# Optimization experiments

Measured on AMD Instinct MI355X. Metric: run time of the kernel, lower is better.

The kernel has to match this reference:

```python
import jax, jax.numpy as jnp
import numpy as np
from jax import lax

V, B, C, H, W, D, G_DEF = 5, 2, 32, 128, 160, 32, 8


def _combine(proj):
    # proj: [B,2,4,4]; [:,0]=extrinsic, [:,1]=intrinsic; new[:, :3, :4] = K[:3,:3] @ E[:3,:4]
    ext, K = proj[:, 0], proj[:, 1]
    top = jnp.einsum('bij,bjk->bik', K[:, :3, :3], ext[:, :3, :4])
    return ext.at[:, :3, :4].set(top)


def _bilinear(img, x, y):
    # img [C,H,W]; x,y [N] pixel coords; zeros padding, align_corners=True (torch grid_sample)
    Ch, Hh, Wh = img.shape
    x0 = jnp.floor(x); y0 = jnp.floor(y)
    wx1 = x - x0; wy1 = y - y0
    def gather(xi, yi):
        valid = ((xi >= 0) & (xi <= Wh - 1) & (yi >= 0) & (yi <= Hh - 1)).astype(img.dtype)
        xc = jnp.clip(xi, 0, Wh - 1).astype(jnp.int32)
        yc = jnp.clip(yi, 0, Hh - 1).astype(jnp.int32)
        return img[:, yc, xc] * valid
    return (gather(x0, y0) * ((1 - wx1) * (1 - wy1)) + gather(x0 + 1, y0) * (wx1 * (1 - wy1))
            + gather(x0, y0 + 1) * ((1 - wx1) * wy1) + gather(x0 + 1, y0 + 1) * (wx1 * wy1))


def _conv3d(x, w, b, pad):
    y = lax.conv_general_dilated(x, w, (1, 1, 1), [(pad, pad)] * 3,
                                 dimension_numbers=('NCDHW', 'OIDHW', 'NCDHW'))
    return y + b[None, :, None, None, None]


def setup_inputs():
    key = jax.random.key(0)
    ks = jax.random.split(key, 8)
    features = jax.random.normal(ks[0], (V, B, C, H, W), jnp.float32)
    pm = np.zeros((B, V, 2, 4, 4), np.float32)
    for v in range(V):
        E = np.eye(4, dtype=np.float32); E[0, 3] = 0.05 * v  # small baseline along x
        K = np.eye(4, dtype=np.float32)
        K[0, 0] = K[1, 1] = float(W); K[0, 2] = W / 2.0; K[1, 2] = H / 2.0
        pm[:, v, 0] = E; pm[:, v, 1] = K
    proj_matrices = jnp.asarray(pm)
    d = jnp.linspace(1.0, 3.0, D, dtype=jnp.float32)
    depth_values = jnp.broadcast_to(d[None, :, None, None], (B, D, H, W))
    s = 0.1
    reg_w1 = jax.random.normal(ks[1], (8, G_DEF, 3, 3, 3), jnp.float32) * s
    reg_b1 = jnp.zeros((8,), jnp.float32)
    reg_w2 = jax.random.normal(ks[2], (1, 8, 3, 3, 3), jnp.float32) * s
    reg_b2 = jnp.zeros((1,), jnp.float32)
    pw_w1 = jax.random.normal(ks[3], (16, 1, 1, 1, 1), jnp.float32) * s
    pw_b1 = jnp.zeros((16,), jnp.float32)
    pw_w2 = jax.random.normal(ks[4], (8, 16, 1, 1, 1), jnp.float32) * s
    pw_b2 = jnp.zeros((8,), jnp.float32)
    pw_w3 = jax.random.normal(ks[5], (1, 8, 1, 1, 1), jnp.float32) * s
    pw_b3 = jnp.zeros((1,), jnp.float32)
    return dict(features=features, proj_matrices=proj_matrices, depth_values=depth_values,
                reg_w1=reg_w1, reg_b1=reg_b1, reg_w2=reg_w2, reg_b2=reg_b2,
                pw_w1=pw_w1, pw_b1=pw_b1, pw_w2=pw_w2, pw_b2=pw_b2,
                pw_w3=pw_w3, pw_b3=pw_b3, num_depth=D, G=G_DEF)


def reference(features, proj_matrices, depth_values, reg_w1, reg_b1, reg_w2, reg_b2,
              pw_w1, pw_b1, pw_w2, pw_b2, pw_w3, pw_b3, num_depth, G):
    Vn, Bn, Cn, Hn, Wn = features.shape
    Dn = num_depth
    ref_fea = features[0].reshape(Bn, G, Cn // G, Hn, Wn)
    ref_proj = _combine(proj_matrices[:, 0])
    ref_proj_inv = jnp.linalg.inv(ref_proj)
    ys, xs = jnp.meshgrid(jnp.arange(Hn, dtype=jnp.float32), jnp.arange(Wn, dtype=jnp.float32), indexing='ij')
    xyz = jnp.stack([xs.ravel(), ys.ravel(), jnp.ones(Hn * Wn, jnp.float32)], 0)  # [3, HW]
    sim_sum = 0.0; w_sum = 0.0; vws = []
    for v in range(1, Vn):  # fixed small view loop
        proj = jnp.einsum('bij,bjk->bik', _combine(proj_matrices[:, v]), ref_proj_inv)
        rot_xyz = jnp.einsum('bij,jn->bin', proj[:, :3, :3], xyz)  # [B,3,HW]
        pxyz = rot_xyz[:, :, None, :] * depth_values.reshape(Bn, 1, Dn, Hn * Wn) \
               + proj[:, :3, 3][:, :, None, None]  # [B,3,D,HW]
        # grid is computed under no_grad in torch -> stop_gradient
        x = lax.stop_gradient((pxyz[:, 0] / pxyz[:, 2]).reshape(Bn, -1))
        y = lax.stop_gradient((pxyz[:, 1] / pxyz[:, 2]).reshape(Bn, -1))
        warped = jax.vmap(_bilinear)(features[v], x, y).reshape(Bn, G, Cn // G, Dn, Hn, Wn)
        sim = (warped * ref_fea[:, :, :, None]).mean(2)  # [B,G,D,H,W] group correlation
        p = jax.nn.softmax(lax.stop_gradient(sim), axis=1)  # detached in torch
        ent = -(p * jnp.log(p + 1e-7)).sum(1, keepdims=True)  # [B,1,D,H,W]
        h = jax.nn.relu(_conv3d(ent, pw_w1, pw_b1, 0))
        h = jax.nn.relu(_conv3d(h, pw_w2, pw_b2, 0))
        vw = jax.nn.sigmoid(_conv3d(h, pw_w3, pw_b3, 0)).max(axis=2)  # [B,1,H,W]
        vws.append(vw)
        sim_sum = sim_sum + sim * vw[:, None]  # broadcast [B,1,1,H,W]
        w_sum = w_sum + vw[:, None]
    view_weights = jnp.concatenate(vws, axis=1)  # [B,V-1,H,W]
    similarity = sim_sum / (w_sum + 1e-6)
    h = jax.nn.relu(_conv3d(similarity, reg_w1, reg_b1, 1))
    prob_volume_pre = _conv3d(h, reg_w2, reg_b2, 1)[:, 0]  # [B,D,H,W]
    prob_volume = jax.nn.softmax(prob_volume_pre, axis=1)
    depth = (prob_volume * depth_values).sum(1)  # [B,H,W]
    pv = lax.stop_gradient(prob_volume)
    padded = jnp.pad(pv, ((0, 0), (1, 2), (0, 0), (0, 0)))
    # 4 * avg_pool3d(kernel=(4,1,1)) == sliding window sum over depth
    sum4 = lax.reduce_window(padded, 0.0, lax.add, (1, 4, 1, 1), (1, 1, 1, 1), 'VALID')
    didx = jnp.clip((pv * jnp.arange(Dn, dtype=pv.dtype)[None, :, None, None]).sum(1).astype(jnp.int32), 0, Dn - 1)
    photometric_confidence = jnp.take_along_axis(sum4, didx[:, None], axis=1)[:, 0]
    return depth, photometric_confidence, view_weights, prob_volume_pre, similarity
```

## Files before the change

### kernel.cpp

```cpp
#include <hip/hip_runtime.h>
#include <hip/hip_bf16.h>
#include <hip/hip_fp16.h>

#define V_  5
#define B_  2
#define C_  32
#define H_  128
#define W_  160
#define D_  32
#define G_  8
#define HW_  (H_*W_)
#define DHW_ (D_*HW_)

#define LOG2E_ 1.4426950408889634f
#define LN2_   0.6931471805599453f
#define LN8_   2.0794415416798357f

typedef _Float16 h8 __attribute__((ext_vector_type(8)));
typedef _Float16 h4 __attribute__((ext_vector_type(4)));
typedef _Float16 h2 __attribute__((ext_vector_type(2)));
typedef float    f4 __attribute__((ext_vector_type(4)));

__device__ inline float fdot2f(h2 a, h2 b, float c) {
#if __has_builtin(__builtin_amdgcn_fdot2)
    return __builtin_amdgcn_fdot2(a, b, c, false);
#else
    return fmaf((float)a[0], (float)b[0], fmaf((float)a[1], (float)b[1], c));
#endif
}



__device__ inline void combine_mat(const float* m, float out[4][4]) {
    const float* ext = m;
    const float* K   = m + 16;
    for (int r = 0; r < 4; ++r)
        for (int c = 0; c < 4; ++c)
            out[r][c] = ext[r*4 + c];
    for (int r = 0; r < 3; ++r)
        for (int c = 0; c < 4; ++c) {
            float s = 0.f;
            for (int k = 0; k < 3; ++k) s += K[r*4 + k] * ext[k*4 + c];
            out[r][c] = s;
        }
}

__device__ inline void invert4(const float Ain[4][4], float Inv[4][4]) {
    float A[4][4];
    for (int r = 0; r < 4; ++r)
        for (int c = 0; c < 4; ++c) {
            A[r][c]   = Ain[r][c];
            Inv[r][c] = (r == c) ? 1.f : 0.f;
        }
    for (int k = 0; k < 4; ++k) {
        int p = k; float best = fabsf(A[k][k]);
        for (int r = k + 1; r < 4; ++r) {
            float v = fabsf(A[r][k]);
            if (v > best) { best = v; p = r; }
        }
        if (p != k) {
            for (int j = 0; j < 4; ++j) {
                float t = A[k][j]; A[k][j] = A[p][j]; A[p][j] = t;
                t = Inv[k][j]; Inv[k][j] = Inv[p][j]; Inv[p][j] = t;
            }
        }
        float dinv = 1.f / A[k][k];
        for (int j = 0; j < 4; ++j) { A[k][j] *= dinv; Inv[k][j] *= dinv; }
        for (int r = 0; r < 4; ++r) {
            if (r == k) continue;
            float f = A[r][k];
            for (int j = 0; j < 4; ++j) {
                A[r][j]  -= f * A[k][j];
                Inv[r][j] -= f * Inv[k][j];
            }
        }
    }
}

__global__ __launch_bounds__(1024) void k_proj(
    const float* __restrict__ pm,
    const float* __restrict__ pw_w1, const float* __restrict__ pw_b1,
    const float* __restrict__ pw_w2, const float* __restrict__ pw_b2,
    const float* __restrict__ pw_w3, const float* __restrict__ pw_b3,
    const float* __restrict__ reg_w1, const float* __restrict__ reg_w2,
    float* __restrict__ proj_ws, float* __restrict__ tabw,
    _Float16* __restrict__ wh1, _Float16* __restrict__ wh2)
{
    int tid = threadIdx.x;
    if (tid < B_) {
        int b = tid;
        float C0[4][4], C0inv[4][4];
        combine_mat(pm + (b * V_ + 0) * 32, C0);
        invert4(C0, C0inv);
        for (int v = 1; v < V_; ++v) {
            float Cv[4][4];
            combine_mat(pm + (b * V_ + v) * 32, Cv);
            float* o = proj_ws + (b * 4 + (v - 1)) * 12;
            for (int r = 0; r < 3; ++r)
                for (int c = 0; c < 4; ++c) {
                    float s = 0.f;
                    for (int k = 0; k < 4; ++k) s += Cv[r][k] * C0inv[k][c];
                    o[r*4 + c] = s;
                }
        }
    }
    for (int i = tid; i < 28*16*8; i += 1024) {
        int ic = i & 7; int m = (i >> 3) & 15; int tap = i >> 7;
        wh1[i] = (_Float16)((tap < 27 && m < 8) ? reg_w1[(m*8 + ic)*27 + tap] : 0.f);
        wh2[i] = (_Float16)((tap < 27 && m == 0) ? reg_w2[ic*27 + tap] : 0.f);
    }
    float ent = (float)tid * (LN8_ / 1023.0f);
    float h2v[8];
    #pragma unroll
    for (int j = 0; j < 8; ++j) h2v[j] = pw_b2[j];
    for (int k = 0; k < 16; ++k) {
        float h1 = fmaxf(ent * pw_w1[k] + pw_b1[k], 0.f);
        #pragma unroll
        for (int j = 0; j < 8; ++j) h2v[j] += pw_w2[j*16 + k] * h1;
    }
    float o3 = pw_b3[0];
    #pragma unroll
    for (int j = 0; j < 8; ++j) o3 += pw_w3[j] * fmaxf(h2v[j], 0.f);
    tabw[tid] = 1.f / (1.f + expf(-o3));
}

__global__ __launch_bounds__(1024) void k_transpose(
    const float* __restrict__ in, _Float16* __restrict__ out)
{
    __shared__ float s[32][33];
    const int tx = threadIdx.x, ty = threadIdx.y;
    const int tid = ty * 32 + tx;
    const int hw0 = blockIdx.x * 32;
    const int vb  = blockIdx.y;
    s[ty][tx] = in[(vb * 32 + ty) * HW_ + hw0 + tx];
    __syncthreads();
    if (tid < 256) {
        int hw = tid >> 3, q = tid & 7;
        h4 hv;
        #pragma unroll
        for (int i = 0; i < 4; ++i) hv[i] = (_Float16)s[q*4 + i][hw];
        *(h4*)(out + ((size_t)vb * HW_ + hw0 + hw) * 32 + q*4) = hv;
    }
}

__global__ __launch_bounds__(1024) void k_main(
    const _Float16* __restrict__ featT,
    const float* __restrict__ depthv,
    const float* __restrict__ proj_ws,
    const float* __restrict__ tabw,
    float* __restrict__ out_vw,
    float* __restrict__ out_sim,
    _Float16* __restrict__ simh)
{
    const int tid = threadIdx.x;
    const int wv   = tid >> 6;
    const int lane = tid & 63;
    const int j    = lane >> 5;
    const int d    = lane & 31;
    const int pxl  = wv * 2 + j;
    const int w0 = blockIdx.x * 32;
    const int h  = blockIdx.y;
    const int b  = blockIdx.z;
    const int w  = w0 + pxl;
    const int p  = h * W_ + w;

    __shared__ float tab_s[1024];
    __shared__ float proj_s[48];
    __shared__ float s_sim[G_][32][33];

    tab_s[tid] = tabw[tid];
    if (tid < 48) proj_s[tid] = proj_ws[b * 48 + tid];
    __syncthreads();

    const h8* rp = (const h8*)(featT + ((size_t)b * HW_ + p) * 32);
    h8 r8[4];
    #pragma unroll
    for (int cc = 0; cc < 4; ++cc) r8[cc] = rp[cc];

    const float depth = depthv[(b * D_ + d) * HW_ + p];
    const float xf = (float)w, yf = (float)h;

    float simsum[G_];
    #pragma unroll
    for (int g = 0; g < G_; ++g) simsum[g] = 0.f;
    float wsum = 0.f;

    for (int v = 1; v < V_; ++v) {
        const float* P = &proj_s[(v - 1) * 12];
        float px = (P[0]*xf + P[1]*yf + P[2])  * depth + P[3];
        float py = (P[4]*xf + P[5]*yf + P[6])  * depth + P[7];
        float pz = (P[8]*xf + P[9]*yf + P[10]) * depth + P[11];
        float rz = __builtin_amdgcn_rcpf(pz);
        float xs = px * rz;
        float ys = py * rz;

        float xr = rintf(xs);
        float yr = rintf(ys);
        xs = (fabsf(xs - xr) < 1e-4f) ? xr : xs;
        ys = (fabsf(ys - yr) < 1e-4f) ? yr : ys;

        float x0 = floorf(xs), y0 = floorf(ys);
        float wx1 = xs - x0,  wy1 = ys - y0;
        float wx0 = 1.f - wx1, wy0 = 1.f - wy1;

        bool vx0 = (x0 >= 0.f)     && (x0 <= (float)(W_-1));
        bool vx1 = (x0+1.f >= 0.f) && (x0+1.f <= (float)(W_-1));
        bool vy0 = (y0 >= 0.f)     && (y0 <= (float)(H_-1));
        bool vy1 = (y0+1.f >= 0.f) && (y0+1.f <= (float)(H_-1));

        int xc0 = (int)fminf(fmaxf(x0,     0.f), (float)(W_-1));
        int xc1 = (int)fminf(fmaxf(x0+1.f, 0.f), (float)(W_-1));
        int yc0 = (int)fminf(fmaxf(y0,     0.f), (float)(H_-1));
        int yc1 = (int)fminf(fmaxf(y0+1.f, 0.f), (float)(H_-1));

        float w00 = (vx0 && vy0) ? (wx0 * wy0) : 0.f;
        float w01 = (vx1 && vy0) ? (wx1 * wy0) : 0.f;
        float w10 = (vx0 && vy1) ? (wx0 * wy1) : 0.f;
        float w11 = (vx1 && vy1) ? (wx1 * wy1) : 0.f;

        const _Float16* vbp = featT + (size_t)(v * B_ + b) * HW_ * 32;

        float sim[G_];
        #pragma unroll
        for (int g = 0; g < G_; ++g) sim[g] = 0.f;

        bool top = __any(w00 > 0.f || w01 > 0.f);
        bool bot = __any(w10 > 0.f || w11 > 0.f);

        if (top) {
            h2 w00h = { (_Float16)w00, (_Float16)w00 };
            h2 w01h = { (_Float16)w01, (_Float16)w01 };
            const h8* t00 = (const h8*)(vbp + (size_t)(yc0 * W_ + xc0) * 32);
            const h8* t01 = (const h8*)(vbp + (size_t)(yc0 * W_ + xc1) * 32);
            #pragma unroll
            for (int cc = 0; cc < 4; ++cc) {
                h8 a = t00[cc], bb = t01[cc];
                const h2* ap = (const h2*)&a;
                const h2* bp = (const h2*)&bb;
                const h2* rv2 = (const h2*)&r8[cc];
                #pragma unroll
                for (int jp = 0; jp < 4; ++jp) {
                    h2 fv = ap[jp] * w00h + bp[jp] * w01h;
                    int g = cc*2 + (jp >> 1);
                    sim[g] = fdot2f(fv, rv2[jp], sim[g]);
                }
            }
        }
        if (bot) {
            h2 w10h = { (_Float16)w10, (_Float16)w10 };
            h2 w11h = { (_Float16)w11, (_Float16)w11 };
            const h8* t10 = (const h8*)(vbp + (size_t)(yc1 * W_ + xc0) * 32);
            const h8* t11 = (const h8*)(vbp + (size_t)(yc1 * W_ + xc1) * 32);
            #pragma unroll
            for (int cc = 0; cc < 4; ++cc) {
                h8 cq = t10[cc], dq = t11[cc];
                const h2* cp = (const h2*)&cq;
                const h2* dp = (const h2*)&dq;
                const h2* rv2 = (const h2*)&r8[cc];
                #pragma unroll
                for (int jp = 0; jp < 4; ++jp) {
                    h2 fv = cp[jp] * w10h + dp[jp] * w11h;
                    int g = cc*2 + (jp >> 1);
                    sim[g] = fdot2f(fv, rv2[jp], sim[g]);
                }
            }
        }

        #pragma unroll
        for (int g = 0; g < G_; ++g) sim[g] *= 0.25f;

        float m = sim[0];
        #pragma unroll
        for (int g = 1; g < G_; ++g) m = fmaxf(m, sim[g]);
        float es = 0.f, edot = 0.f;
        #pragma unroll
        for (int g = 0; g < G_; ++g) {
            float e = exp2f((sim[g] - m) * LOG2E_);
            es += e;
            edot = fmaf(e, sim[g], edot);
        }
        float inv_es = __builtin_amdgcn_rcpf(es);
        float ent = m + log2f(es) * LN2_ - edot * inv_es;

        float t = ent * (1023.0f / LN8_);
        t = fminf(fmaxf(t, 0.f), 1022.999f);
        int it = (int)t;
        float fr = t - (float)it;
        float lo = tab_s[it], hi = tab_s[it + 1];
        float sig = fmaf(hi - lo, fr, lo);

        float mv = sig;
        #pragma unroll
        for (int k = 16; k >= 1; k >>= 1)
            mv = fmaxf(mv, __shfl_xor(mv, k, 64));
        if (d == 0)
            out_vw[(b * 4 + (v - 1)) * HW_ + p] = mv;

        #pragma unroll
        for (int g = 0; g < G_; ++g) simsum[g] = fmaf(sim[g], mv, simsum[g]);
        wsum += mv;
    }

    float wn = __builtin_amdgcn_rcpf(wsum + 1e-6f);
    #pragma unroll
    for (int g = 0; g < G_; ++g) s_sim[g][d][pxl] = simsum[g] * wn;
    __syncthreads();

    const int tx = tid & 31;
    const int ty = tid >> 5;
    float* so = out_sim + (size_t)b * G_ * DHW_ + ty * HW_ + h * W_ + w0 + tx;
    h8 hv;
    #pragma unroll
    for (int g = 0; g < G_; ++g) {
        float val = s_sim[g][ty][tx];
        so[(size_t)g * DHW_] = val;
        hv[g] = (_Float16)val;
    }
    *(h8*)(simh + ((size_t)(b * D_ + ty) * HW_ + h * W_ + w0 + tx) * 8) = hv;
}


__global__ __launch_bounds__(256) void k_conv1m(
    const _Float16* __restrict__ in,
    const _Float16* __restrict__ wh,
    const float* __restrict__ bias,
    _Float16* __restrict__ outh)
{
    __shared__ _Float16 halo[6*10*34*8];
    const int tid = threadIdx.x;
    const int w0 = blockIdx.x * 32;
    const int h0 = blockIdx.y * 8;
    const int z  = blockIdx.z;
    const int b  = z >> 3;
    const int d0 = (z & 7) * 4;

    for (int pos = tid; pos < 2040; pos += 256) {
        int wx = pos % 34; int r = pos / 34; int hy = r % 10; int dz = r / 10;
        int gw = w0 + wx - 1, gh = h0 + hy - 1, gd = d0 + dz - 1;
        uint4 val = make_uint4(0u, 0u, 0u, 0u);
        if (gw >= 0 && gw < W_ && gh >= 0 && gh < H_ && gd >= 0 && gd < D_)
            val = *(const uint4*)(in + (((size_t)(b*D_ + gd)*H_ + gh)*W_ + gw)*8);
        *(uint4*)(halo + pos*8) = val;
    }

    const int wave = tid >> 6, lane = tid & 63;
    const int n = lane & 15, quad = lane >> 4;

    h8 afrag[7];
    int chunkoff[7];
    #pragma unroll
    for (int c = 0; c < 7; ++c) {
        int tap = c*4 + quad;
        afrag[c] = *(const h8*)(wh + (tap*16 + n)*8);
        int tapc = tap > 26 ? 26 : tap;
        int dz = tapc / 9; int rem = tapc - dz*9;
        int hyo = rem / 3; int wxo = rem - hyo*3;
        chunkoff[c] = ((dz*10 + hyo)*34 + wxo)*8;
    }
    f4 binit;
    #pragma unroll
    for (int reg = 0; reg < 4; ++reg)
        binit[reg] = (quad < 2) ? bias[quad*4 + reg] : 0.f;

    __syncthreads();

    #pragma unroll
    for (int it = 0; it < 4; ++it) {
        int t = wave*4 + it;
        int h_row = t >> 1, whalf = t & 1;
        int tileoff = (h_row*34 + whalf*16 + n)*8;
        #pragma unroll
        for (int dout = 0; dout < 4; ++dout) {
            f4 acc = binit;
            #pragma unroll
            for (int c = 0; c < 7; ++c) {
                h8 bfrag = *(const h8*)(halo + chunkoff[c] + dout*2720 + tileoff);
                acc = __builtin_amdgcn_mfma_f32_16x16x32_f16(afrag[c], bfrag, acc, 0, 0, 0);
            }
            if (quad < 2) {
                h4 hv;
                #pragma unroll
                for (int reg = 0; reg < 4; ++reg) hv[reg] = (_Float16)fmaxf(acc[reg], 0.f);
                *(h4*)(outh + (((size_t)(b*D_ + d0 + dout)*H_ + h0 + h_row)*W_ + w0 + whalf*16 + n)*8 + quad*4) = hv;
            }
        }
    }
}

__global__ __launch_bounds__(256) void k_conv2m(
    const _Float16* __restrict__ in,
    const _Float16* __restrict__ wh,
    const float* __restrict__ bias,
    float* __restrict__ out)
{
    __shared__ _Float16 halo[6*10*34*8];
    const int tid = threadIdx.x;
    const int w0 = blockIdx.x * 32;
    const int h0 = blockIdx.y * 8;
    const int z  = blockIdx.z;
    const int b  = z >> 3;
    const int d0 = (z & 7) * 4;

    for (int pos = tid; pos < 2040; pos += 256) {
        int wx = pos % 34; int r = pos / 34; int hy = r % 10; int dz = r / 10;
        int gw = w0 + wx - 1, gh = h0 + hy - 1, gd = d0 + dz - 1;
        uint4 val = make_uint4(0u, 0u, 0u, 0u);
        if (gw >= 0 && gw < W_ && gh >= 0 && gh < H_ && gd >= 0 && gd < D_)
            val = *(const uint4*)(in + (((size_t)(b*D_ + gd)*H_ + gh)*W_ + gw)*8);
        *(uint4*)(halo + pos*8) = val;
    }

    const int wave = tid >> 6, lane = tid & 63;
    const int n = lane & 15, quad = lane >> 4;

    h8 afrag[7];
    int chunkoff[7];
    #pragma unroll
    for (int c = 0; c < 7; ++c) {
        int tap = c*4 + quad;
        afrag[c] = *(const h8*)(wh + (tap*16 + n)*8);
        int tapc = tap > 26 ? 26 : tap;
        int dz = tapc / 9; int rem = tapc - dz*9;
        int hyo = rem / 3; int wxo = rem - hyo*3;
        chunkoff[c] = ((dz*10 + hyo)*34 + wxo)*8;
    }
    const float b0 = bias[0];

    __syncthreads();

    #pragma unroll
    for (int it = 0; it < 4; ++it) {
        int t = wave*4 + it;
        int h_row = t >> 1, whalf = t & 1;
        int tileoff = (h_row*34 + whalf*16 + n)*8;
        #pragma unroll
        for (int dout = 0; dout < 4; ++dout) {
            f4 acc;
            acc[0] = (quad == 0) ? b0 : 0.f;
            acc[1] = 0.f; acc[2] = 0.f; acc[3] = 0.f;
            #pragma unroll
            for (int c = 0; c < 7; ++c) {
                h8 bfrag = *(const h8*)(halo + chunkoff[c] + dout*2720 + tileoff);
                acc = __builtin_amdgcn_mfma_f32_16x16x32_f16(afrag[c], bfrag, acc, 0, 0, 0);
            }
            if (quad == 0)
                out[(((size_t)(b*D_ + d0 + dout)*H_ + h0 + h_row)*W_ + w0 + whalf*16 + n)] = acc[0];
        }
    }
}

__global__ __launch_bounds__(256) void k_final(
    const float* __restrict__ pvp,
    const float* __restrict__ depthv,
    float* __restrict__ out_depth,
    float* __restrict__ out_conf)
{
    int i = blockIdx.x * 256 + threadIdx.x;
    if (i >= B_ * HW_) return;
    int b = i / HW_;
    int p = i - b * HW_;

    const float* pp = pvp + b * DHW_ + p;
    const float* dv = depthv + b * DHW_ + p;

    float x[D_];
    float m = -3.4e38f;
    #pragma unroll
    for (int d = 0; d < D_; ++d) { x[d] = pp[d * HW_]; m = fmaxf(m, x[d]); }
    float s = 0.f;
    #pragma unroll
    for (int d = 0; d < D_; ++d) { x[d] = exp2f((x[d] - m) * LOG2E_); s += x[d]; }
    float inv = 1.f / s;

    float dep = 0.f, fd = 0.f;
    #pragma unroll
    for (int d = 0; d < D_; ++d) {
        float pv = x[d] * inv;
        x[d] = pv;
        dep = fmaf(pv, dv[d * HW_], dep);
        fd  = fmaf(pv, (float)d, fd);
    }
    int di = (int)fd;
    di = di < 0 ? 0 : (di > D_ - 1 ? D_ - 1 : di);
    float conf = 0.f;
    #pragma unroll
    for (int k = 0; k < 4; ++k) {
        int idx = di - 1 + k;
        if (idx >= 0 && idx < D_) conf += x[idx];
    }
    out_depth[i] = dep;
    out_conf[i]  = conf;
}

extern "C" void kernel_launch(void* const* d_in, const int* in_sizes, int n_in,
                              void* d_out, int out_size, void* d_ws, size_t ws_size,
                              hipStream_t stream) {
    const float* feat   = (const float*)d_in[0];
    const float* pm     = (const float*)d_in[1];
    const float* depthv = (const float*)d_in[2];
    const float* reg_w1 = (const float*)d_in[3];
    const float* reg_b1 = (const float*)d_in[4];
    const float* reg_w2 = (const float*)d_in[5];
    const float* reg_b2 = (const float*)d_in[6];
    const float* pw_w1  = (const float*)d_in[7];
    const float* pw_b1  = (const float*)d_in[8];
    const float* pw_w2  = (const float*)d_in[9];
    const float* pw_b2  = (const float*)d_in[10];
    const float* pw_w3  = (const float*)d_in[11];
    const float* pw_b3  = (const float*)d_in[12];

    float* out = (float*)d_out;
    float* out_depth = out;
    float* out_conf  = out + B_*HW_;
    float* out_vw    = out + 2*B_*HW_;
    float* out_pvp   = out_vw + B_*4*HW_;
    float* out_sim   = out_pvp + B_*DHW_;

    float* ws      = (float*)d_ws;
    float* proj_ws = ws;
    float* tabw    = ws + 128;
    _Float16* wh1  = (_Float16*)(ws + 1152);
    _Float16* wh2  = (_Float16*)(ws + 2944);
    _Float16* featT = (_Float16*)(ws + 4736);
    _Float16* hidh  = (_Float16*)(ws + 4736);
    _Float16* simh  = (_Float16*)(ws + 4736 + 5242880);

    hipLaunchKernelGGL(k_proj, dim3(1), dim3(1024), 0, stream,
                       pm, pw_w1, pw_b1, pw_w2, pw_b2, pw_w3, pw_b3,
                       reg_w1, reg_w2, proj_ws, tabw, wh1, wh2);

    hipLaunchKernelGGL(k_transpose, dim3(HW_/32, V_*B_), dim3(32, 32), 0, stream,
                       feat, featT);

    hipLaunchKernelGGL(k_main, dim3(W_/32, H_, B_), dim3(1024), 0, stream,
                       featT, depthv, proj_ws, tabw, out_vw, out_sim, simh);

    hipLaunchKernelGGL(k_conv1m, dim3(W_/32, H_/8, B_*D_/4), dim3(256), 0, stream,
                       simh, wh1, reg_b1, hidh);

    hipLaunchKernelGGL(k_conv2m, dim3(W_/32, H_/8, B_*D_/4), dim3(256), 0, stream,
                       hidh, wh2, reg_b2, out_pvp);

    hipLaunchKernelGGL(k_final, dim3((B_*HW_ + 255)/256), dim3(256), 0, stream,
                       out_pvp, depthv, out_depth, out_conf);
}
```

Before: 213.5 us.

## Remap k_main threads to pixel-major lanes with shared-memory depth max reduction

```diff
diff --git a/kernel.cpp b/kernel.cpp
--- a/kernel.cpp
+++ b/kernel.cpp
@@ -152,32 +152,33 @@
     float* __restrict__ out_sim,
     _Float16* __restrict__ simh)
 {
-    const int tid = threadIdx.x;
+    const int tid  = threadIdx.x;
+    const int px   = tid & 31;
+    const int d    = tid >> 5;
     const int wv   = tid >> 6;
     const int lane = tid & 63;
-    const int j    = lane >> 5;
-    const int d    = lane & 31;
-    const int pxl  = wv * 2 + j;
     const int w0 = blockIdx.x * 32;
     const int h  = blockIdx.y;
     const int b  = blockIdx.z;
-    const int w  = w0 + pxl;
+    const int w  = w0 + px;
     const int p  = h * W_ + w;
 
     __shared__ float tab_s[1024];
     __shared__ float proj_s[48];
-    __shared__ float s_sim[G_][32][33];
+    __shared__ float s_red[4][16][32];
 
     tab_s[tid] = tabw[tid];
     if (tid < 48) proj_s[tid] = proj_ws[b * 48 + tid];
     __syncthreads();
 
-    const h8* rp = (const h8*)(featT + ((size_t)b * HW_ + p) * 32);
+    const char* refbase = (const char*)(featT + (size_t)b * HW_ * 32);
+    const uint32_t refoff = (uint32_t)p * 64u;
     h8 r8[4];
     #pragma unroll
-    for (int cc = 0; cc < 4; ++cc) r8[cc] = rp[cc];
-
-    const float depth = depthv[(b * D_ + d) * HW_ + p];
+    for (int cc = 0; cc < 4; ++cc)
+        r8[cc] = *(const h8*)(refbase + refoff + cc * 16);
+
+    const float depth = depthv[(uint32_t)(b * D_ + d) * HW_ + (uint32_t)p];
     const float xf = (float)w, yf = (float)h;
 
     float simsum[G_];
@@ -185,14 +186,15 @@
     for (int g = 0; g < G_; ++g) simsum[g] = 0.f;
     float wsum = 0.f;
 
+    #pragma unroll
     for (int v = 1; v < V_; ++v) {
         const float* P = &proj_s[(v - 1) * 12];
-        float px = (P[0]*xf + P[1]*yf + P[2])  * depth + P[3];
-        float py = (P[4]*xf + P[5]*yf + P[6])  * depth + P[7];
-        float pz = (P[8]*xf + P[9]*yf + P[10]) * depth + P[11];
-        float rz = __builtin_amdgcn_rcpf(pz);
-        float xs = px * rz;
-        float ys = py * rz;
+        float px_ = (P[0]*xf + P[1]*yf + P[2])  * depth + P[3];
+        float py_ = (P[4]*xf + P[5]*yf + P[6])  * depth + P[7];
+        float pz_ = (P[8]*xf + P[9]*yf + P[10]) * depth + P[11];
+        float rz = __builtin_amdgcn_rcpf(pz_);
+        float xs = px_ * rz;
+        float ys = py_ * rz;
 
         float xr = rintf(xs);
         float yr = rintf(ys);
@@ -218,7 +220,11 @@
         float w10 = (vx0 && vy1) ? (wx0 * wy1) : 0.f;
         float w11 = (vx1 && vy1) ? (wx1 * wy1) : 0.f;
 
-        const _Float16* vbp = featT + (size_t)(v * B_ + b) * HW_ * 32;
+        const char* vbp = (const char*)(featT + (size_t)(v * B_ + b) * HW_ * 32);
+        uint32_t o00 = ((uint32_t)(yc0 * W_ + xc0)) * 64u;
+        uint32_t o01 = ((uint32_t)(yc0 * W_ + xc1)) * 64u;
+        uint32_t o10 = ((uint32_t)(yc1 * W_ + xc0)) * 64u;
+        uint32_t o11 = ((uint32_t)(yc1 * W_ + xc1)) * 64u;
 
         float sim[G_];
         #pragma unroll
@@ -230,11 +236,10 @@
         if (top) {
             h2 w00h = { (_Float16)w00, (_Float16)w00 };
             h2 w01h = { (_Float16)w01, (_Float16)w01 };
-            const h8* t00 = (const h8*)(vbp + (size_t)(yc0 * W_ + xc0) * 32);
-            const h8* t01 = (const h8*)(vbp + (size_t)(yc0 * W_ + xc1) * 32);
             #pragma unroll
             for (int cc = 0; cc < 4; ++cc) {
-                h8 a = t00[cc], bb = t01[cc];
+                h8 a  = *(const h8*)(vbp + o00 + cc * 16);
+                h8 bb = *(const h8*)(vbp + o01 + cc * 16);
                 const h2* ap = (const h2*)&a;
                 const h2* bp = (const h2*)&bb;
                 const h2* rv2 = (const h2*)&r8[cc];
@@ -249,11 +254,10 @@
         if (bot) {
             h2 w10h = { (_Float16)w10, (_Float16)w10 };
             h2 w11h = { (_Float16)w11, (_Float16)w11 };
-            const h8* t10 = (const h8*)(vbp + (size_t)(yc1 * W_ + xc0) * 32);
-            const h8* t11 = (const h8*)(vbp + (size_t)(yc1 * W_ + xc1) * 32);
             #pragma unroll
             for (int cc = 0; cc < 4; ++cc) {
-                h8 cq = t10[cc], dq = t11[cc];
+                h8 cq = *(const h8*)(vbp + o10 + cc * 16);
+                h8 dq = *(const h8*)(vbp + o11 + cc * 16);
                 const h2* cp = (const h2*)&cq;
                 const h2* dp = (const h2*)&dq;
                 const h2* rv2 = (const h2*)&r8[cc];
@@ -289,11 +293,13 @@
         float lo = tab_s[it], hi = tab_s[it + 1];
         float sig = fmaf(hi - lo, fr, lo);
 
-        float mv = sig;
-        #pragma unroll
-        for (int k = 16; k >= 1; k >>= 1)
-            mv = fmaxf(mv, __shfl_xor(mv, k, 64));
-        if (d == 0)
+        float m2 = fmaxf(sig, __shfl_xor(sig, 32, 64));
+        if (lane < 32) s_red[v - 1][wv][px] = m2;
+        __syncthreads();
+        float mv = s_red[v - 1][0][px];
+        #pragma unroll
+        for (int k = 1; k < 16; ++k) mv = fmaxf(mv, s_red[v - 1][k][px]);
+        if (tid < 32)
             out_vw[(b * 4 + (v - 1)) * HW_ + p] = mv;
 
         #pragma unroll
@@ -302,21 +308,15 @@
     }
 
     float wn = __builtin_amdgcn_rcpf(wsum + 1e-6f);
-    #pragma unroll
-    for (int g = 0; g < G_; ++g) s_sim[g][d][pxl] = simsum[g] * wn;
-    __syncthreads();
-
-    const int tx = tid & 31;
-    const int ty = tid >> 5;
-    float* so = out_sim + (size_t)b * G_ * DHW_ + ty * HW_ + h * W_ + w0 + tx;
+    float* so = out_sim + (size_t)b * G_ * DHW_ + (size_t)d * HW_ + p;
     h8 hv;
     #pragma unroll
     for (int g = 0; g < G_; ++g) {
-        float val = s_sim[g][ty][tx];
+        float val = simsum[g] * wn;
         so[(size_t)g * DHW_] = val;
         hv[g] = (_Float16)val;
     }
-    *(h8*)(simh + ((size_t)(b * D_ + ty) * HW_ + h * W_ + w0 + tx) * 8) = hv;
+    *(h8*)(simh + ((size_t)(b * D_ + d) * HW_ + p) * 8) = hv;
 }
 
 
```

Measured after the change: 224.4 us. 5.1% more time.
